# Kernel optimization log

Hardware: AMD Instinct MI355X
Metric: run time of the kernel (lower is better)

Reference implementation:

```python
import jax, jax.numpy as jnp
import numpy as np

B = 16           # batch graphs
C = 2            # canonical orderings
STEPS = 64       # subgraphs (generation steps) per ordering
NUM_SUB = B * C * STEPS          # 2048 segments
EDGES_PER_SUB = 1024
E = NUM_SUB * EDGES_PER_SUB      # 2,097,152 augmented edges
K = 20                           # mixture components
POS_WEIGHT = 1.0                 # BCEWithLogitsLoss pos_weight (edge_weight)


def setup_inputs() -> dict:
    key = jax.random.key(0)
    k1, k2, k3 = jax.random.split(key, 3)
    label = jax.random.bernoulli(k1, 0.3, (E,)).astype(jnp.float32)
    log_theta = jax.random.normal(k2, (E, K), dtype=jnp.float32)
    log_alpha = jax.random.normal(k3, (E, K), dtype=jnp.float32)
    subgraph_idx = jnp.repeat(jnp.arange(NUM_SUB, dtype=jnp.int32), EDGES_PER_SUB)
    # cumulative subgraph counts per batch graph (C*STEPS subgraphs each)
    subgraph_idx_base = jnp.arange(B + 1, dtype=jnp.int32) * (C * STEPS)
    return {
        "label": label,
        "log_theta": log_theta,
        "log_alpha": log_alpha,
        "subgraph_idx": subgraph_idx,
        "subgraph_idx_base": subgraph_idx_base,
        "num_canonical_order": C,
        "num_subgraph": NUM_SUB,
    }


def _bce_with_logits(x, y):
    # torch BCEWithLogitsLoss(pos_weight=w, reduction='none')
    return POS_WEIGHT * y * jax.nn.softplus(-x) + (1.0 - y) * jax.nn.softplus(x)


def _mixture_bernoulli_loss(label, log_theta, log_alpha, subgraph_idx,
                            subgraph_idx_base, C, num_subgraph):
    nB = subgraph_idx_base.shape[0] - 1
    seg = subgraph_idx.astype(jnp.int32)

    # per-edge, per-component BCE nll: [E, K]
    adj_nll = _bce_with_logits(log_theta, label[:, None])
    # mask out last edge of each subgraph segment
    mask = jnp.concatenate([seg[:-1] == seg[1:], jnp.array([False])])
    adj_nll = adj_nll * mask[:, None].astype(adj_nll.dtype)

    ones_e = jnp.ones_like(label)
    num_edges_per_subgraph = jax.ops.segment_sum(ones_e, seg, num_segments=num_subgraph)
    reduce_adj_nll = jax.ops.segment_sum(adj_nll, seg, num_segments=num_subgraph)
    reduce_log_alpha = jax.ops.segment_sum(log_alpha, seg, num_segments=num_subgraph)
    reduce_log_alpha = reduce_log_alpha / num_edges_per_subgraph[:, None]
    reduce_log_alpha = jax.nn.log_softmax(reduce_log_alpha, axis=-1)

    # mixture log-likelihood per subgraph: [num_subgraph]
    log_prob = jax.scipy.special.logsumexp(-reduce_adj_nll + reduce_log_alpha, axis=1)

    # map each subgraph -> (graph, ordering) bucket index in [0, B*C)
    s = jnp.arange(num_subgraph, dtype=jnp.int32)
    b = jnp.searchsorted(subgraph_idx_base, s, side="right").astype(jnp.int32) - 1
    per_batch = subgraph_idx_base[b + 1] - subgraph_idx_base[b]
    bc_size = per_batch // C
    bc_idx = b * C + (s - subgraph_idx_base[b]) // bc_size

    bc_log_prob = jax.ops.segment_sum(log_prob, bc_idx, num_segments=nB * C)
    bc_const = jax.ops.segment_sum(num_edges_per_subgraph, bc_idx, num_segments=nB * C)
    bc_loss = (bc_log_prob / bc_const).reshape(nB, C)
    bc_log_prob = bc_log_prob.reshape(nB, C)

    b_log_prob = jax.scipy.special.logsumexp(bc_log_prob, axis=1)
    b_loss = jax.scipy.special.logsumexp(bc_loss, axis=1)

    b_loss = -b_loss
    rewards = jnp.ones(nB, dtype=b_loss.dtype)  # rewards=None path, baseline=0
    pos_loss = b_loss * rewards * (rewards > 0).astype(b_loss.dtype)
    neg_loss = jnp.log(1.0 - jnp.exp(-b_loss) + 1e-6) * rewards * (rewards < 0).astype(b_loss.dtype)
    loss = neg_loss + pos_loss
    return loss.mean()  # reduction='mean'


def reference(label, log_theta, log_alpha, subgraph_idx, subgraph_idx_base,
              num_canonical_order, num_subgraph):
    return _mixture_bernoulli_loss(label, log_theta, log_alpha, subgraph_idx,
                                   subgraph_idx_base, num_canonical_order,
                                   num_subgraph)
```

## Files before the change

### kernel.cpp

```cpp
#include <hip/hip_runtime.h>
#include <hip/hip_bf16.h>
#include <math.h>

#define KC 20
#define EPS 1024
#define NUM_SUB 2048
#define NBUCKET 32
#define SUBS_PER_BUCKET 64
#define NB 16

__global__ __launch_bounds__(320) void gran_pass1(
    const float* __restrict__ label,
    const float* __restrict__ log_theta,
    const float* __restrict__ log_alpha,
    float* __restrict__ log_prob_out)
{
    const int s = blockIdx.x;
    const int t = threadIdx.x;
    const int q = t / 5;

    const long base_e  = (long)s * EPS;
    const long base_p4 = (long)s * (EPS * KC / 4) + t;

    const float4* __restrict__ th4 = (const float4*)log_theta;
    const float4* __restrict__ al4 = (const float4*)log_alpha;

    float y[16];
#pragma unroll
    for (int m = 0; m < 16; ++m) y[m] = label[base_e + q + 64 * m];

    float accT[4] = {0.f, 0.f, 0.f, 0.f};
    float accA[4] = {0.f, 0.f, 0.f, 0.f};

#pragma unroll
    for (int mb = 0; mb < 16; mb += 4) {
        float4 th[4], al[4];
#pragma unroll
        for (int u = 0; u < 4; ++u) {
            th[u] = th4[base_p4 + 320 * (mb + u)];
            al[u] = al4[base_p4 + 320 * (mb + u)];
        }
#pragma unroll
        for (int u = 0; u < 4; ++u) {
            const int   m   = mb + u;
            const int   e   = q + 64 * m;
            const float msk = (e != EPS - 1) ? 1.f : 0.f;
            const float yy  = y[m];
            const float xs[4] = {th[u].x, th[u].y, th[u].z, th[u].w};
            const float av[4] = {al[u].x, al[u].y, al[u].z, al[u].w};
#pragma unroll
            for (int c = 0; c < 4; ++c) {
                const float x = xs[c];
                const float sp  = __logf(1.0f + __expf(-fabsf(x)));
                const float bce = fmaxf(x, 0.f) - yy * x + sp;
                accT[c] += msk * bce;
                accA[c] += av[c];
            }
        }
    }

    __shared__ float sT[320][4];
    __shared__ float sA[320][4];
#pragma unroll
    for (int c = 0; c < 4; ++c) { sT[t][c] = accT[c]; sA[t][c] = accA[c]; }
    __syncthreads();

    __shared__ float rT[KC];
    __shared__ float rA[KC];
    if (t < KC) {
        const int jj = t >> 2;
        const int cc = t & 3;
        float st = 0.f, sa = 0.f;
        for (int qq = 0; qq < 64; ++qq) {
            st += sT[5 * qq + jj][cc];
            sa += sA[5 * qq + jj][cc];
        }
        rT[t] = st;
        rA[t] = sa * (1.0f / EPS);
    }
    __syncthreads();

    if (t == 0) {
        float vT[KC], vA[KC];
#pragma unroll
        for (int k = 0; k < KC; ++k) { vT[k] = rT[k]; vA[k] = rA[k]; }
        float mx = vA[0];
#pragma unroll
        for (int k = 1; k < KC; ++k) mx = fmaxf(mx, vA[k]);
        float sum = 0.f;
#pragma unroll
        for (int k = 0; k < KC; ++k) sum += expf(vA[k] - mx);
        const float lse = mx + logf(sum);
        float M = -3.4e38f;
        float v[KC];
#pragma unroll
        for (int k = 0; k < KC; ++k) { v[k] = vA[k] - lse - vT[k]; M = fmaxf(M, v[k]); }
        float s2 = 0.f;
#pragma unroll
        for (int k = 0; k < KC; ++k) s2 += expf(v[k] - M);
        log_prob_out[s] = M + logf(s2);
    }
}

__global__ __launch_bounds__(64) void gran_pass2(
    const float* __restrict__ log_prob, float* __restrict__ out)
{
    const int t = threadIdx.x;
    __shared__ double bc_loss[NBUCKET];
    if (t < NBUCKET) {
        double sum = 0.0;
        const float* p = log_prob + (long)t * SUBS_PER_BUCKET;
        for (int i = 0; i < SUBS_PER_BUCKET; ++i) sum += (double)p[i];
        bc_loss[t] = sum / (double)(SUBS_PER_BUCKET * EPS);
    }
    __syncthreads();
    if (t == 0) {
        double total = 0.0;
        for (int b = 0; b < NB; ++b) {
            const double a = bc_loss[2 * b];
            const double c = bc_loss[2 * b + 1];
            const double m = fmax(a, c);
            const float  ea = __expf((float)(a - m));
            const float  ec = __expf((float)(c - m));
            const double lse = m + (double)logf(ea + ec);
            total += -lse;
        }
        out[0] = (float)(total / (double)NB);
    }
}

extern "C" void kernel_launch(void* const* d_in, const int* in_sizes, int n_in,
                              void* d_out, int out_size, void* d_ws, size_t ws_size,
                              hipStream_t stream) {
    const float* label     = (const float*)d_in[0];
    const float* log_theta = (const float*)d_in[1];
    const float* log_alpha = (const float*)d_in[2];

    float* log_prob = (float*)d_ws;
    float* out      = (float*)d_out;

    gran_pass1<<<NUM_SUB, 320, 0, stream>>>(label, log_theta, log_alpha, log_prob);
    gran_pass2<<<1, 64, 0, stream>>>(log_prob, out);
}
```

Before: 360.9 us.

## Split each subgraph across two blocks and move mixture logsumexp to separate kernel

The streaming pass now uses 4096 blocks, each covering half a subgraph. Each block writes per-component partial sums of the BCE and log_alpha terms to workspace, and a new small kernel combines the halves and computes the per-subgraph log-softmax/logsumexp. The in-block reduction is reorganized so all 320 threads do a first-level sum instead of 20 threads looping over 64 entries, and the serial single-thread epilogue is removed from the bandwidth-bound kernel. The final reduction kernel is also widened to 256 threads. This trades more parallelism and shorter block tails for an extra launch and some additional workspace traffic.

```diff
diff --git a/kernel.cpp b/kernel.cpp
--- a/kernel.cpp
+++ b/kernel.cpp
@@ -8,32 +8,35 @@
 #define NBUCKET 32
 #define SUBS_PER_BUCKET 64
 #define NB 16
+#define NBLK1 4096
+#define HALF 512
 
-__global__ __launch_bounds__(320) void gran_pass1(
+__global__ __launch_bounds__(320, 6) void gran_pass1a(
     const float* __restrict__ label,
     const float* __restrict__ log_theta,
     const float* __restrict__ log_alpha,
-    float* __restrict__ log_prob_out)
+    float* __restrict__ pT,
+    float* __restrict__ pA)
 {
-    const int s = blockIdx.x;
+    const int h = blockIdx.x;
     const int t = threadIdx.x;
     const int q = t / 5;
 
-    const long base_e  = (long)s * EPS;
-    const long base_p4 = (long)s * (EPS * KC / 4) + t;
+    const long base_e  = (long)h * HALF;
+    const long base_p4 = (long)h * (HALF * KC / 4) + t;
 
     const float4* __restrict__ th4 = (const float4*)log_theta;
     const float4* __restrict__ al4 = (const float4*)log_alpha;
 
-    float y[16];
+    float y[8];
 #pragma unroll
-    for (int m = 0; m < 16; ++m) y[m] = label[base_e + q + 64 * m];
+    for (int m = 0; m < 8; ++m) y[m] = label[base_e + q + 64 * m];
 
     float accT[4] = {0.f, 0.f, 0.f, 0.f};
     float accA[4] = {0.f, 0.f, 0.f, 0.f};
 
 #pragma unroll
-    for (int mb = 0; mb < 16; mb += 4) {
+    for (int mb = 0; mb < 8; mb += 4) {
         float4 th[4], al[4];
 #pragma unroll
         for (int u = 0; u < 4; ++u) {
@@ -43,8 +46,8 @@
 #pragma unroll
         for (int u = 0; u < 4; ++u) {
             const int   m   = mb + u;
-            const int   e   = q + 64 * m;
-            const float msk = (e != EPS - 1) ? 1.f : 0.f;
+            const int   le  = q + 64 * m;
+            const float msk = (((h & 1) == 1) && (le == HALF - 1)) ? 0.f : 1.f;
             const float yy  = y[m];
             const float xs[4] = {th[u].x, th[u].y, th[u].z, th[u].w};
             const float av[4] = {al[u].x, al[u].y, al[u].z, al[u].w};
@@ -59,59 +62,86 @@
         }
     }
 
-    __shared__ float sT[320][4];
-    __shared__ float sA[320][4];
+    __shared__ float sT[320 * 4];
+    __shared__ float sA[320 * 4];
 #pragma unroll
-    for (int c = 0; c < 4; ++c) { sT[t][c] = accT[c]; sA[t][c] = accA[c]; }
+    for (int c = 0; c < 4; ++c) { sT[t * 4 + c] = accT[c]; sA[t * 4 + c] = accA[c]; }
     __syncthreads();
 
-    __shared__ float rT[KC];
-    __shared__ float rA[KC];
-    if (t < KC) {
-        const int jj = t >> 2;
-        const int cc = t & 3;
+    __shared__ float mT[16 * KC];
+    __shared__ float mA[16 * KC];
+    {
         float st = 0.f, sa = 0.f;
-        for (int qq = 0; qq < 64; ++qq) {
-            st += sT[5 * qq + jj][cc];
-            sa += sA[5 * qq + jj][cc];
-        }
-        rT[t] = st;
-        rA[t] = sa * (1.0f / EPS);
+#pragma unroll
+        for (int i = 0; i < 4; ++i) { st += sT[t + 320 * i]; sa += sA[t + 320 * i]; }
+        mT[t] = st;
+        mA[t] = sa;
     }
     __syncthreads();
 
-    if (t == 0) {
-        float vT[KC], vA[KC];
+    if (t < KC) {
+        float st = 0.f, sa = 0.f;
 #pragma unroll
-        for (int k = 0; k < KC; ++k) { vT[k] = rT[k]; vA[k] = rA[k]; }
-        float mx = vA[0];
-#pragma unroll
-        for (int k = 1; k < KC; ++k) mx = fmaxf(mx, vA[k]);
-        float sum = 0.f;
-#pragma unroll
-        for (int k = 0; k < KC; ++k) sum += expf(vA[k] - mx);
-        const float lse = mx + logf(sum);
-        float M = -3.4e38f;
-        float v[KC];
-#pragma unroll
-        for (int k = 0; k < KC; ++k) { v[k] = vA[k] - lse - vT[k]; M = fmaxf(M, v[k]); }
-        float s2 = 0.f;
-#pragma unroll
-        for (int k = 0; k < KC; ++k) s2 += expf(v[k] - M);
-        log_prob_out[s] = M + logf(s2);
+        for (int g = 0; g < 16; ++g) { st += mT[g * KC + t]; sa += mA[g * KC + t]; }
+        pT[(long)h * KC + t] = st;
+        pA[(long)h * KC + t] = sa;
     }
 }
 
-__global__ __launch_bounds__(64) void gran_pass2(
+__global__ __launch_bounds__(256) void gran_pass1b(
+    const float* __restrict__ pT,
+    const float* __restrict__ pA,
+    float* __restrict__ log_prob_out)
+{
+    const int s = blockIdx.x * 256 + threadIdx.x;
+    if (s >= NUM_SUB) return;
+    const long b0 = (long)(2 * s) * KC;
+    const long b1 = (long)(2 * s + 1) * KC;
+
+    float vT[KC], vA[KC];
+#pragma unroll
+    for (int k = 0; k < KC; ++k) {
+        vT[k] = pT[b0 + k] + pT[b1 + k];
+        vA[k] = (pA[b0 + k] + pA[b1 + k]) * (1.0f / EPS);
+    }
+    float mx = vA[0];
+#pragma unroll
+    for (int k = 1; k < KC; ++k) mx = fmaxf(mx, vA[k]);
+    float sum = 0.f;
+#pragma unroll
+    for (int k = 0; k < KC; ++k) sum += expf(vA[k] - mx);
+    const float lse = mx + logf(sum);
+    float M = -3.4e38f;
+    float v[KC];
+#pragma unroll
+    for (int k = 0; k < KC; ++k) { v[k] = vA[k] - lse - vT[k]; M = fmaxf(M, v[k]); }
+    float s2 = 0.f;
+#pragma unroll
+    for (int k = 0; k < KC; ++k) s2 += expf(v[k] - M);
+    log_prob_out[s] = M + logf(s2);
+}
+
+__global__ __launch_bounds__(256) void gran_pass2(
     const float* __restrict__ log_prob, float* __restrict__ out)
 {
     const int t = threadIdx.x;
+    const int bucket = t >> 3;
+    const int r      = t & 7;
+    double s = 0.0;
+    const float* p = log_prob + (long)bucket * SUBS_PER_BUCKET + r * 8;
+#pragma unroll
+    for (int i = 0; i < 8; ++i) s += (double)p[i];
+
+    __shared__ double part[256];
+    part[t] = s;
+    __syncthreads();
+
     __shared__ double bc_loss[NBUCKET];
     if (t < NBUCKET) {
-        double sum = 0.0;
-        const float* p = log_prob + (long)t * SUBS_PER_BUCKET;
-        for (int i = 0; i < SUBS_PER_BUCKET; ++i) sum += (double)p[i];
-        bc_loss[t] = sum / (double)(SUBS_PER_BUCKET * EPS);
+        double b = 0.0;
+#pragma unroll
+        for (int rr = 0; rr < 8; ++rr) b += part[t * 8 + rr];
+        bc_loss[t] = b / (double)(SUBS_PER_BUCKET * EPS);
     }
     __syncthreads();
     if (t == 0) {
@@ -120,10 +150,8 @@
             const double a = bc_loss[2 * b];
             const double c = bc_loss[2 * b + 1];
             const double m = fmax(a, c);
-            const float  ea = __expf((float)(a - m));
-            const float  ec = __expf((float)(c - m));
-            const double lse = m + (double)logf(ea + ec);
-            total += -lse;
+            const double lsv = m + log(exp(a - m) + exp(c - m));
+            total += -lsv;
         }
         out[0] = (float)(total / (double)NB);
     }
@@ -136,9 +164,12 @@
     const float* log_theta = (const float*)d_in[1];
     const float* log_alpha = (const float*)d_in[2];
 
-    float* log_prob = (float*)d_ws;
+    float* pT       = (float*)d_ws;
+    float* pA       = pT + (long)NBLK1 * KC;
+    float* log_prob = pA + (long)NBLK1 * KC;
     float* out      = (float*)d_out;
 
-    gran_pass1<<<NUM_SUB, 320, 0, stream>>>(label, log_theta, log_alpha, log_prob);
-    gran_pass2<<<1, 64, 0, stream>>>(log_prob, out);
+    gran_pass1a<<<NBLK1, 320, 0, stream>>>(label, log_theta, log_alpha, pT, pA);
+    gran_pass1b<<<(NUM_SUB + 255) / 256, 256, 0, stream>>>(pT, pA, log_prob);
+    gran_pass2<<<1, 256, 0, stream>>>(log_prob, out);
 }
```

After: 360.6 us. Within noise of the previous version (-0.1%).
